# Performance work log

Measured on AMD Instinct MI355X. Metric: run time of the kernel, lower is better.

## Reference

```python
import jax, jax.numpy as jnp
import numpy as np
import math

D = 1024
H = 16
HD = D // H
P = 64  # bias_proj_dim
B, N, M = 4, 1024, 2048
EPS_LN = 1e-5
EPS_NORM = 1e-12


def _ln(x, g, b):
    mu = jnp.mean(x, axis=-1, keepdims=True)
    var = jnp.var(x, axis=-1, keepdims=True)
    return (x - mu) * jax.lax.rsqrt(var + EPS_LN) * g + b


def _l2norm_dim1(x):
    # torch F.normalize(x, p=2) default dim=1 -> normalize over the sequence axis
    n = jnp.sqrt(jnp.sum(x * x, axis=1, keepdims=True))
    return x / jnp.maximum(n, EPS_NORM)


def setup_inputs() -> dict:
    key = jax.random.key(0)
    ks = jax.random.split(key, 16)
    s = 1.0 / math.sqrt(D)
    inp = {
        'dataset_features': jax.random.normal(ks[0], (B, N, D), jnp.float32),
        'visual_features': jax.random.normal(ks[1], (B, M, D), jnp.float32),
        # linear weights stored as (in, out): y = x @ W + b
        'wq_w': jax.random.normal(ks[2], (D, D), jnp.float32) * s,
        'wq_b': jnp.zeros((D,), jnp.float32),
        'wk_w': jax.random.normal(ks[3], (D, D), jnp.float32) * s,
        'wk_b': jnp.zeros((D,), jnp.float32),
        'wv_w': jax.random.normal(ks[4], (D, D), jnp.float32) * s,
        'wv_b': jnp.zeros((D,), jnp.float32),
        'wo_w': jax.random.normal(ks[5], (D, D), jnp.float32) * s,
        'wo_b': jnp.zeros((D,), jnp.float32),
        'gq_w': jax.random.normal(ks[6], (D, P), jnp.float32) * s,
        'gq_b': jnp.zeros((P,), jnp.float32),
        'gk_w': jax.random.normal(ks[7], (D, P), jnp.float32) * s,
        'gk_b': jnp.zeros((P,), jnp.float32),
        'pos_scale': jnp.asarray(2.0, jnp.float32),
        'neg_scale': jnp.asarray(50.0, jnp.float32),
        'attn_logit_scale': jnp.asarray(math.log(10.0), jnp.float32),
        'ln_q_g': jnp.ones((D,), jnp.float32),
        'ln_q_b': jnp.zeros((D,), jnp.float32),
        'ln_kv_g': jnp.ones((D,), jnp.float32),
        'ln_kv_b': jnp.zeros((D,), jnp.float32),
        'ln_out_g': jnp.ones((D,), jnp.float32),
        'ln_out_b': jnp.zeros((D,), jnp.float32),
        'ff1_w': jax.random.normal(ks[8], (D, 2 * D), jnp.float32) * s,
        'ff1_b': jnp.zeros((2 * D,), jnp.float32),
        'ff2_w': jax.random.normal(ks[9], (2 * D, D), jnp.float32) * (1.0 / math.sqrt(2 * D)),
        'ff2_b': jnp.zeros((D,), jnp.float32),
    }
    return inp


def reference(dataset_features, visual_features, wq_w, wq_b, wk_w, wk_b, wv_w, wv_b,
              wo_w, wo_b, gq_w, gq_b, gk_w, gk_b, pos_scale, neg_scale,
              attn_logit_scale, ln_q_g, ln_q_b, ln_kv_g, ln_kv_b, ln_out_g, ln_out_b,
              ff1_w, ff1_b, ff2_w, ff2_b):
    residual = dataset_features
    q_in = _ln(dataset_features, ln_q_g, ln_q_b)   # [B,N,D]
    kv_in = _ln(visual_features, ln_kv_g, ln_kv_b)  # [B,M,D]

    geo_q = _l2norm_dim1(q_in @ gq_w + gq_b)   # [B,N,P], normalized over N
    geo_k = _l2norm_dim1(kv_in @ gk_w + gk_b)  # [B,M,P], normalized over M
    bias_raw = jnp.einsum('bnp,bmp->bnm', geo_q, geo_k)  # [B,N,M]
    full_bias = jax.nn.relu(bias_raw) * pos_scale - jax.nn.relu(-bias_raw) * neg_scale

    q = (q_in @ wq_w + wq_b).reshape(B, N, H, HD).transpose(0, 2, 1, 3)   # [B,H,N,hd]
    k = (kv_in @ wk_w + wk_b).reshape(B, M, H, HD).transpose(0, 2, 1, 3)  # [B,H,M,hd]
    v = (kv_in @ wv_w + wv_b).reshape(B, M, H, HD).transpose(0, 2, 1, 3)

    logits = jnp.einsum('bhnd,bhmd->bhnm', q, k) / math.sqrt(HD)
    logits = logits * jnp.exp(attn_logit_scale)
    scores = logits + full_bias[:, None, :, :]
    attn = jax.nn.softmax(scores, axis=-1)
    out = jnp.einsum('bhnm,bhmd->bhnd', attn, v).transpose(0, 2, 1, 3).reshape(B, N, D)
    out = out @ wo_w + wo_b
    out = residual + out

    residual = out
    h = _ln(out, ln_out_g, ln_out_b)
    ff = jax.nn.gelu(h @ ff1_w + ff1_b, approximate=False) @ ff2_w + ff2_b
    return residual + ff
```

## Files before the change

### kernel.cpp

```cpp
#include <hip/hip_runtime.h>


typedef __bf16 bf16x8 __attribute__((ext_vector_type(8)));
typedef float  f32x4  __attribute__((ext_vector_type(4)));

__device__ inline f32x4 mfma16(bf16x8 a, bf16x8 b, f32x4 c) {
  return __builtin_amdgcn_mfma_f32_16x16x32_bf16(a, b, c, 0, 0, 0);
}

__device__ inline void glds16(const void* g, void* l) {
  __builtin_amdgcn_global_load_lds(
      (const __attribute__((address_space(1))) void*)g,
      (__attribute__((address_space(3))) void*)l, 16, 0, 0);
}

__device__ inline int swz(int row, int col) {
  return row * 64 + ((((col >> 3) ^ (row & 7)) << 3) | (col & 7));
}

#define DB 1024
#define DH 16
#define DHD 64
#define DP 64
#define NB 4
#define NN 1024
#define NM 2048

__global__ __launch_bounds__(256) void k_transpose_all(
    const float* __restrict__ w0, const float* __restrict__ w1,
    const float* __restrict__ w2, const float* __restrict__ w3,
    const float* __restrict__ f1, const float* __restrict__ f2,
    const float* __restrict__ g0, const float* __restrict__ g1,
    __bf16* __restrict__ o0, __bf16* __restrict__ o1,
    __bf16* __restrict__ o2, __bf16* __restrict__ o3,
    __bf16* __restrict__ of1, __bf16* __restrict__ of2,
    __bf16* __restrict__ og0, __bf16* __restrict__ og1) {
  __shared__ float tile[32][33];
  int id = blockIdx.x;
  const float* in;
  __bf16* out;
  int K, O, x, y;
  if (id < 4096) {
    int mi = id >> 10, r = id & 1023;
    in = mi == 0 ? w0 : mi == 1 ? w1 : mi == 2 ? w2 : w3;
    out = mi == 0 ? o0 : mi == 1 ? o1 : mi == 2 ? o2 : o3;
    K = 1024; O = 1024; x = r & 31; y = r >> 5;
  } else if (id < 6144) {
    int r = id - 4096; in = f1; out = of1; K = 1024; O = 2048; x = r & 63; y = r >> 6;
  } else if (id < 8192) {
    int r = id - 6144; in = f2; out = of2; K = 2048; O = 1024; x = r & 31; y = r >> 5;
  } else if (id < 8256) {
    int r = id - 8192; in = g0; out = og0; K = 1024; O = 64; x = r & 1; y = r >> 1;
  } else {
    int r = id - 8256; in = g1; out = og1; K = 1024; O = 64; x = r & 1; y = r >> 1;
  }
  int k0 = y * 32, o0c = x * 32;
  int tx = threadIdx.x & 31, ty = threadIdx.x >> 5;
#pragma unroll
  for (int r = ty; r < 32; r += 8)
    tile[r][tx] = in[(size_t)(k0 + r) * O + (o0c + tx)];
  __syncthreads();
#pragma unroll
  for (int r = ty; r < 32; r += 8)
    out[(size_t)(o0c + r) * K + (k0 + tx)] = (__bf16)tile[tx][r];
}

__device__ inline void ln_body(const float* __restrict__ x,
                               const float* __restrict__ g,
                               const float* __restrict__ bb,
                               __bf16* __restrict__ y, size_t row) {
  int t = threadIdx.x;
  float4 v = ((const float4*)(x + row * 1024))[t];
  float s = v.x + v.y + v.z + v.w;
  float ss = v.x * v.x + v.y * v.y + v.z * v.z + v.w * v.w;
#pragma unroll
  for (int o = 32; o; o >>= 1) {
    s += __shfl_down(s, o, 64);
    ss += __shfl_down(ss, o, 64);
  }
  __shared__ float r1[4], r2[4];
  if ((t & 63) == 0) { r1[t >> 6] = s; r2[t >> 6] = ss; }
  __syncthreads();
  s = r1[0] + r1[1] + r1[2] + r1[3];
  ss = r2[0] + r2[1] + r2[2] + r2[3];
  float mu = s * (1.f / 1024.f);
  float rstd = rsqrtf(ss * (1.f / 1024.f) - mu * mu + 1e-5f);
  float4 gv = ((const float4*)g)[t];
  float4 bv = ((const float4*)bb)[t];
  __bf16* yr = y + row * 1024 + t * 4;
  yr[0] = (__bf16)((v.x - mu) * rstd * gv.x + bv.x);
  yr[1] = (__bf16)((v.y - mu) * rstd * gv.y + bv.y);
  yr[2] = (__bf16)((v.z - mu) * rstd * gv.z + bv.z);
  yr[3] = (__bf16)((v.w - mu) * rstd * gv.w + bv.w);
}

__global__ __launch_bounds__(256) void k_layernorm(
    const float* __restrict__ x, const float* __restrict__ g,
    const float* __restrict__ bb, __bf16* __restrict__ y) {
  ln_body(x, g, bb, y, blockIdx.x);
}

__global__ __launch_bounds__(256) void k_layernorm2(
    const float* __restrict__ x1, const float* __restrict__ g1,
    const float* __restrict__ b1, __bf16* __restrict__ y1,
    const float* __restrict__ x2, const float* __restrict__ g2,
    const float* __restrict__ b2, __bf16* __restrict__ y2) {
  int row = blockIdx.x;
  if (row < 4096) ln_body(x1, g1, b1, y1, row);
  else ln_body(x2, g2, b2, y2, row - 4096);
}

__global__ __launch_bounds__(256) void k_geo(
    const __bf16* __restrict__ qin, const __bf16* __restrict__ kvin,
    const __bf16* __restrict__ gqw, const __bf16* __restrict__ gkw,
    const float* __restrict__ gqb, const float* __restrict__ gkb,
    __bf16* __restrict__ geoq, __bf16* __restrict__ geok) {
  const int blk = blockIdx.x;
  const bool isq = blk < 128;
  const __bf16* A = isq ? qin : kvin;
  const __bf16* Bt = isq ? gqw : gkw;
  const float* bias = isq ? gqb : gkb;
  __bf16* C = isq ? geoq : geok;
  const int row0 = (isq ? blk : blk - 128) * 32;
  __shared__ __align__(16) __bf16 As[32][72], Bs[64][72];
  const int t = threadIdx.x, lane = t & 63, w = t >> 6;
  const int quad = lane >> 4, l15 = lane & 15;
  const int wr = w >> 1, wc = w & 1;
  const int sr = t >> 3, skc = (t & 7) * 8;
  const __bf16* aP = A + (size_t)(row0 + sr) * 1024 + skc;
  const __bf16* bP0 = Bt + (size_t)sr * 1024 + skc;
  const __bf16* bP1 = Bt + (size_t)(sr + 32) * 1024 + skc;
  bf16x8 av = *(const bf16x8*)aP;
  bf16x8 bv0 = *(const bf16x8*)bP0;
  bf16x8 bv1 = *(const bf16x8*)bP1;
  f32x4 acc[2] = {};
  for (int k0 = 0; k0 < 1024; k0 += 64) {
    __syncthreads();
    *(bf16x8*)&As[sr][skc] = av;
    *(bf16x8*)&Bs[sr][skc] = bv0;
    *(bf16x8*)&Bs[sr + 32][skc] = bv1;
    __syncthreads();
    if (k0 + 64 < 1024) {
      av = *(const bf16x8*)(aP + k0 + 64);
      bv0 = *(const bf16x8*)(bP0 + k0 + 64);
      bv1 = *(const bf16x8*)(bP1 + k0 + 64);
    }
#pragma unroll
    for (int ks = 0; ks < 2; ks++) {
      bf16x8 af = *(const bf16x8*)&As[wr * 16 + l15][ks * 32 + quad * 8];
#pragma unroll
      for (int ct = 0; ct < 2; ct++) {
        bf16x8 bfr = *(const bf16x8*)&Bs[wc * 32 + ct * 16 + l15][ks * 32 + quad * 8];
        acc[ct] = mfma16(af, bfr, acc[ct]);
      }
    }
  }
#pragma unroll
  for (int ct = 0; ct < 2; ct++) {
    int col = wc * 32 + ct * 16 + l15;
    float bc = bias[col];
#pragma unroll
    for (int i = 0; i < 4; i++) {
      int row = row0 + wr * 16 + quad * 4 + i;
      C[(size_t)row * 64 + col] = (__bf16)(acc[ct][i] + bc);
    }
  }
}

__global__ __launch_bounds__(256) void k_l2sum(
    const __bf16* __restrict__ gq, const __bf16* __restrict__ gk,
    float* __restrict__ sums) {
  int chunk = blockIdx.x, b = blockIdx.y, z = blockIdx.z;
  if (z == 0 && chunk >= 8) return;
  const __bf16* src = z ? gk : gq;
  int rows = z ? 2048 : 1024;
  const unsigned* base = (const unsigned*)(src + (size_t)b * rows * 64) + chunk * 128 * 32;
  int t = threadIdx.x, c = t & 31, ro = t >> 5;
  float s0 = 0.f, s1 = 0.f;
  for (int r = ro; r < 128; r += 8) {
    unsigned u = base[r * 32 + c];
    float f0 = __uint_as_float(u << 16);
    float f1 = __uint_as_float(u & 0xffff0000u);
    s0 += f0 * f0;
    s1 += f1 * f1;
  }
  __shared__ float ls[64];
  if (t < 64) ls[t] = 0.f;
  __syncthreads();
  atomicAdd(&ls[c * 2], s0);
  atomicAdd(&ls[c * 2 + 1], s1);
  __syncthreads();
  if (t < 64) atomicAdd(&sums[z * 256 + b * 64 + t], ls[t]);
}

__global__ __launch_bounds__(256) void k_l2scale(
    __bf16* __restrict__ gk, const float* __restrict__ sums) {
  int chunk = blockIdx.x, b = blockIdx.y;
  unsigned* base = (unsigned*)(gk + (size_t)b * 2048 * 64) + chunk * 128 * 32;
  int t = threadIdx.x, c = t & 31, ro = t >> 5;
  float sq0 = sums[b * 64 + c * 2], sq1 = sums[b * 64 + c * 2 + 1];
  float sk0 = sums[256 + b * 64 + c * 2], sk1 = sums[256 + b * 64 + c * 2 + 1];
  float m0 = 1.f / (fmaxf(sqrtf(sq0), 1e-12f) * fmaxf(sqrtf(sk0), 1e-12f));
  float m1 = 1.f / (fmaxf(sqrtf(sq1), 1e-12f) * fmaxf(sqrtf(sk1), 1e-12f));
  for (int r = ro; r < 128; r += 8) {
    unsigned u = base[r * 32 + c];
    float f0 = __uint_as_float(u << 16) * m0;
    float f1 = __uint_as_float(u & 0xffff0000u) * m1;
    unsigned short h0 = __builtin_bit_cast(unsigned short, (__bf16)f0);
    unsigned short h1 = __builtin_bit_cast(unsigned short, (__bf16)f1);
    base[r * 32 + c] = (unsigned)h0 | ((unsigned)h1 << 16);
  }
}

__global__ __launch_bounds__(256, 3) void k_qkv(
    const __bf16* __restrict__ qin, const __bf16* __restrict__ kvin,
    const __bf16* __restrict__ twq, const __bf16* __restrict__ twk,
    const __bf16* __restrict__ twv, const float* __restrict__ qbias,
    const float* __restrict__ kbias, const float* __restrict__ vbias,
    __bf16* __restrict__ qb, __bf16* __restrict__ kb, __bf16* __restrict__ vtb) {
  int id = blockIdx.x;
  const __bf16 *A, *Bt;
  const float* bias;
  __bf16* C;
  int my, nx, Ndim;
  bool rowbias;
  if (id < 256) {
    A = qin; Bt = twq; bias = qbias; C = qb;
    nx = id & 7; my = id >> 3; Ndim = 1024; rowbias = false;
  } else if (id < 768) {
    id -= 256;
    A = kvin; Bt = twk; bias = kbias; C = kb;
    nx = id & 7; my = id >> 3; Ndim = 1024; rowbias = false;
  } else {
    id -= 768;
    A = twv; Bt = kvin; bias = vbias; C = vtb;
    nx = id & 63; my = id >> 6; Ndim = 8192; rowbias = true;
  }
  const int Kdim = 1024;
  __shared__ __align__(16) __bf16 As[128 * 32];
  __shared__ __align__(16) __bf16 Bs[128 * 32];
  const int m0 = my * 128, n0 = nx * 128;
  const int t = threadIdx.x, lane = t & 63, w = t >> 6;
  const int quad = lane >> 4, l15 = lane & 15;
  const int wr = w >> 1, wc = w & 1;
  const int srow = lane >> 2, scol = (lane & 3) * 8;
  const __bf16* aS0 = A + (size_t)(m0 + w * 32 + srow) * Kdim + scol;
  const __bf16* bS0 = Bt + (size_t)(n0 + w * 32 + srow) * Kdim + scol;
  const size_t K16 = (size_t)16 * Kdim;
  __bf16* lA0 = &As[(w * 32) * 32];
  __bf16* lB0 = &Bs[(w * 32) * 32];

  f32x4 acc[4][4] = {};
  for (int k0 = 0; k0 < Kdim; k0 += 32) {
    __syncthreads();
    glds16(aS0 + k0, lA0);
    glds16(aS0 + K16 + k0, lA0 + 16 * 32);
    glds16(bS0 + k0, lB0);
    glds16(bS0 + K16 + k0, lB0 + 16 * 32);
    __syncthreads();
    bf16x8 af[4], bg[4];
#pragma unroll
    for (int rt = 0; rt < 4; rt++)
      af[rt] = *(const bf16x8*)&As[(wr * 64 + rt * 16 + l15) * 32 + quad * 8];
#pragma unroll
    for (int ct = 0; ct < 4; ct++)
      bg[ct] = *(const bf16x8*)&Bs[(wc * 64 + ct * 16 + l15) * 32 + quad * 8];
#pragma unroll
    for (int rt = 0; rt < 4; rt++)
#pragma unroll
      for (int ct = 0; ct < 4; ct++)
        acc[rt][ct] = mfma16(af[rt], bg[ct], acc[rt][ct]);
  }
#pragma unroll
  for (int rt = 0; rt < 4; rt++) {
    int row = m0 + wr * 64 + rt * 16 + quad * 4;
#pragma unroll
    for (int ct = 0; ct < 4; ct++) {
      int col = n0 + wc * 64 + ct * 16 + l15;
      float bcol = rowbias ? 0.f : bias[col];
#pragma unroll
      for (int i = 0; i < 4; i++) {
        float vv = acc[rt][ct][i] + (rowbias ? bias[row + i] : bcol);
        C[(size_t)(row + i) * Ndim + col] = (__bf16)vv;
      }
    }
  }
}

__global__ __launch_bounds__(256, 3) void k_gemm128g(
    const __bf16* __restrict__ A, const __bf16* __restrict__ Bt,
    const float* __restrict__ bias, __bf16* __restrict__ Cout,
    int Ndim, int Kdim) {
  __shared__ __align__(16) __bf16 As[128 * 32];
  __shared__ __align__(16) __bf16 Bs[128 * 32];
  const int m0 = blockIdx.y * 128, n0 = blockIdx.x * 128;
  const int t = threadIdx.x, lane = t & 63, w = t >> 6;
  const int quad = lane >> 4, l15 = lane & 15;
  const int wr = w >> 1, wc = w & 1;
  const int srow = lane >> 2, scol = (lane & 3) * 8;
  const __bf16* aS0 = A + (size_t)(m0 + w * 32 + srow) * Kdim + scol;
  const __bf16* bS0 = Bt + (size_t)(n0 + w * 32 + srow) * Kdim + scol;
  const size_t K16 = (size_t)16 * Kdim;
  __bf16* lA0 = &As[(w * 32) * 32];
  __bf16* lB0 = &Bs[(w * 32) * 32];

  f32x4 acc[4][4] = {};
  for (int k0 = 0; k0 < Kdim; k0 += 32) {
    __syncthreads();
    glds16(aS0 + k0, lA0);
    glds16(aS0 + K16 + k0, lA0 + 16 * 32);
    glds16(bS0 + k0, lB0);
    glds16(bS0 + K16 + k0, lB0 + 16 * 32);
    __syncthreads();
    bf16x8 af[4], bg[4];
#pragma unroll
    for (int rt = 0; rt < 4; rt++)
      af[rt] = *(const bf16x8*)&As[(wr * 64 + rt * 16 + l15) * 32 + quad * 8];
#pragma unroll
    for (int ct = 0; ct < 4; ct++)
      bg[ct] = *(const bf16x8*)&Bs[(wc * 64 + ct * 16 + l15) * 32 + quad * 8];
#pragma unroll
    for (int rt = 0; rt < 4; rt++)
#pragma unroll
      for (int ct = 0; ct < 4; ct++)
        acc[rt][ct] = mfma16(af[rt], bg[ct], acc[rt][ct]);
  }
#pragma unroll
  for (int rt = 0; rt < 4; rt++) {
    int row = m0 + wr * 64 + rt * 16 + quad * 4;
#pragma unroll
    for (int ct = 0; ct < 4; ct++) {
      int col = n0 + wc * 64 + ct * 16 + l15;
      float bcol = bias[col];
#pragma unroll
      for (int i = 0; i < 4; i++) {
        float vv = acc[rt][ct][i] + bcol;
        Cout[(size_t)(row + i) * Ndim + col] =
            (__bf16)(0.5f * vv * (1.f + erff(vv * 0.70710678118f)));
      }
    }
  }
}

__global__ __launch_bounds__(256, 2) void k_gemmn64(
    const __bf16* __restrict__ A, const __bf16* __restrict__ Bt,
    const float* __restrict__ bias, const float* __restrict__ resid,
    float* __restrict__ Cout, int Ndim, int Kdim) {
  __shared__ __align__(16) __bf16 As[128 * 32];
  __shared__ __align__(16) __bf16 Bs[64 * 32];
  const int m0 = blockIdx.y * 128, n0 = blockIdx.x * 64;
  const int t = threadIdx.x, lane = t & 63, w = t >> 6;
  const int quad = lane >> 4, l15 = lane & 15;
  const int wr = w >> 1, wc = w & 1;
  const int srow = lane >> 2, scol = (lane & 3) * 8;
  const __bf16* aS0 = A + (size_t)(m0 + w * 32 + srow) * Kdim + scol;
  const __bf16* bS0 = Bt + (size_t)(n0 + w * 16 + srow) * Kdim + scol;
  const size_t K16 = (size_t)16 * Kdim;
  __bf16* lA0 = &As[(w * 32) * 32];
  __bf16* lB0 = &Bs[(w * 16) * 32];

  f32x4 acc[4][2] = {};
  for (int k0 = 0; k0 < Kdim; k0 += 32) {
    __syncthreads();
    glds16(aS0 + k0, lA0);
    glds16(aS0 + K16 + k0, lA0 + 16 * 32);
    glds16(bS0 + k0, lB0);
    __syncthreads();
    bf16x8 af[4], bg[2];
#pragma unroll
    for (int rt = 0; rt < 4; rt++)
      af[rt] = *(const bf16x8*)&As[(wr * 64 + rt * 16 + l15) * 32 + quad * 8];
#pragma unroll
    for (int ct = 0; ct < 2; ct++)
      bg[ct] = *(const bf16x8*)&Bs[(wc * 32 + ct * 16 + l15) * 32 + quad * 8];
#pragma unroll
    for (int rt = 0; rt < 4; rt++)
#pragma unroll
      for (int ct = 0; ct < 2; ct++)
        acc[rt][ct] = mfma16(af[rt], bg[ct], acc[rt][ct]);
  }
#pragma unroll
  for (int rt = 0; rt < 4; rt++) {
    int row = m0 + wr * 64 + rt * 16 + quad * 4;
#pragma unroll
    for (int ct = 0; ct < 2; ct++) {
      int col = n0 + wc * 32 + ct * 16 + l15;
      float bcol = bias[col];
#pragma unroll
      for (int i = 0; i < 4; i++) {
        size_t idx = (size_t)(row + i) * Ndim + col;
        Cout[idx] = acc[rt][ct][i] + bcol + resid[idx];
      }
    }
  }
}

__global__ __launch_bounds__(256, 2) void k_flash(
    const __bf16* __restrict__ Q, const __bf16* __restrict__ K,
    const __bf16* __restrict__ Vt, const __bf16* __restrict__ Gq,
    const __bf16* __restrict__ Gk, const float* __restrict__ als,
    const float* __restrict__ psc, const float* __restrict__ nsc,
    float* __restrict__ Opart, float* __restrict__ lpart) {
  const int o = blockIdx.x;
  const int bh = o & 63, kv = (o >> 6) & 1, x = o >> 7;
  const int b = bh & 3, h = bh >> 2;
  const int t = threadIdx.x, w = t >> 6, lane = t & 63;
  const int quad = lane >> 4, l15 = lane & 15;
  const int row0 = x * 128 + w * 32;
  const float LOG2E = 1.44269504089f;
  const float sc2 = __expf(als[0]) * 0.125f * LOG2E;
  const float pos2 = psc[0] * LOG2E, neg2 = nsc[0] * LOG2E;

  __shared__ __align__(16) __bf16 Ks[64 * 64];
  __shared__ __align__(16) __bf16 Gs[64 * 64];
  __shared__ __align__(16) __bf16 Vs[64 * 64];
  __shared__ __align__(16) __bf16 plds[4][32 * 64];

  const __bf16* Qb = Q + ((size_t)(b * NN + row0)) * DB + h * DHD;
  const __bf16* Kb = K + ((size_t)b * NM) * DB + h * DHD;
  const __bf16* Vb = Vt + (size_t)(h * DHD) * (NB * NM) + (size_t)b * NM;
  const __bf16* Gqb = Gq + (size_t)(b * NN + row0) * DP;
  const __bf16* Gkb = Gk + (size_t)b * NM * DP;

  const int r0 = t >> 3, ch = t & 7, gc = ch * 8;
  const int sw0 = swz(r0, gc), sw1 = sw0 + 32 * 64;
  const int r1 = r0 + 32;

  bf16x8 qf[2][2], gqf[2][2];
#pragma unroll
  for (int rt = 0; rt < 2; rt++)
#pragma unroll
    for (int ks = 0; ks < 2; ks++) {
      qf[rt][ks] = *(const bf16x8*)(Qb + (size_t)(rt * 16 + l15) * DB + ks * 32 + quad * 8);
      gqf[rt][ks] = *(const bf16x8*)(Gqb + (size_t)(rt * 16 + l15) * DP + ks * 32 + quad * 8);
    }

  const int mlo = kv * 1024;
  bf16x8 kst0 = *(const bf16x8*)(Kb + (size_t)(mlo + r0) * DB + gc);
  bf16x8 kst1 = *(const bf16x8*)(Kb + (size_t)(mlo + r1) * DB + gc);
  bf16x8 gst0 = *(const bf16x8*)(Gkb + (size_t)(mlo + r0) * DP + gc);
  bf16x8 gst1 = *(const bf16x8*)(Gkb + (size_t)(mlo + r1) * DP + gc);
  bf16x8 vst0 = *(const bf16x8*)(Vb + (size_t)r0 * (NB * NM) + mlo + gc);
  bf16x8 vst1 = *(const bf16x8*)(Vb + (size_t)r1 * (NB * NM) + mlo + gc);

  float lrow[2][4] = {};
  f32x4 oacc[2][4] = {};
  f32x4 z4 = {0.f, 0.f, 0.f, 0.f};

  for (int m0 = mlo; m0 < mlo + 1024; m0 += 64) {
    __syncthreads();
    *(bf16x8*)&Ks[sw0] = kst0;
    *(bf16x8*)&Ks[sw1] = kst1;
    *(bf16x8*)&Gs[sw0] = gst0;
    *(bf16x8*)&Gs[sw1] = gst1;
    *(bf16x8*)&Vs[sw0] = vst0;
    *(bf16x8*)&Vs[sw1] = vst1;
    __syncthreads();
    if (m0 + 64 < mlo + 1024) {
      kst0 = *(const bf16x8*)(Kb + (size_t)(m0 + 64 + r0) * DB + gc);
      kst1 = *(const bf16x8*)(Kb + (size_t)(m0 + 64 + r1) * DB + gc);
      gst0 = *(const bf16x8*)(Gkb + (size_t)(m0 + 64 + r0) * DP + gc);
      gst1 = *(const bf16x8*)(Gkb + (size_t)(m0 + 64 + r1) * DP + gc);
      vst0 = *(const bf16x8*)(Vb + (size_t)r0 * (NB * NM) + m0 + 64 + gc);
      vst1 = *(const bf16x8*)(Vb + (size_t)r1 * (NB * NM) + m0 + 64 + gc);
    }
    bf16x8 kf[4][2], gkf[4][2];
#pragma unroll
    for (int ct = 0; ct < 4; ct++)
#pragma unroll
      for (int ks = 0; ks < 2; ks++) {
        int off = swz(ct * 16 + l15, ks * 32 + quad * 8);
        kf[ct][ks] = *(const bf16x8*)&Ks[off];
        gkf[ct][ks] = *(const bf16x8*)&Gs[off];
      }
#pragma unroll
    for (int rt = 0; rt < 2; rt++)
#pragma unroll
      for (int ct = 0; ct < 4; ct++) {
        f32x4 s = mfma16(qf[rt][1], kf[ct][1], mfma16(qf[rt][0], kf[ct][0], z4));
        f32x4 bg = mfma16(gqf[rt][1], gkf[ct][1], mfma16(gqf[rt][0], gkf[ct][0], z4));
#pragma unroll
        for (int i = 0; i < 4; i++) {
          float bb = bg[i];
          float scl = bb > 0.f ? pos2 : neg2;
          float p = __builtin_amdgcn_exp2f(fmaf(bb, scl, s[i] * sc2));
          lrow[rt][i] += p;
          plds[w][swz(rt * 16 + quad * 4 + i, ct * 16 + l15)] = (__bf16)p;
        }
      }
    bf16x8 pf[2][2], vf[4][2];
#pragma unroll
    for (int rt = 0; rt < 2; rt++)
#pragma unroll
      for (int ms = 0; ms < 2; ms++)
        pf[rt][ms] = *(const bf16x8*)&plds[w][swz(rt * 16 + l15, ms * 32 + quad * 8)];
#pragma unroll
    for (int dt = 0; dt < 4; dt++)
#pragma unroll
      for (int ms = 0; ms < 2; ms++)
        vf[dt][ms] = *(const bf16x8*)&Vs[swz(dt * 16 + l15, ms * 32 + quad * 8)];
#pragma unroll
    for (int rt = 0; rt < 2; rt++)
#pragma unroll
      for (int dt = 0; dt < 4; dt++) {
        oacc[rt][dt] = mfma16(pf[rt][0], vf[dt][0], oacc[rt][dt]);
        oacc[rt][dt] = mfma16(pf[rt][1], vf[dt][1], oacc[rt][dt]);
      }
  }
  float* op = Opart + ((size_t)kv * NB * NN + b * NN + row0) * DB + h * 64;
  float* lp = lpart + ((size_t)kv * NB * NN + b * NN + row0) * DH + h;
#pragma unroll
  for (int rt = 0; rt < 2; rt++)
#pragma unroll
    for (int i = 0; i < 4; i++) {
      float l = lrow[rt][i];
#pragma unroll
      for (int o2 = 1; o2 < 16; o2 <<= 1) l += __shfl_xor(l, o2, 64);
      int r = rt * 16 + quad * 4 + i;
#pragma unroll
      for (int dt = 0; dt < 4; dt++)
        op[(size_t)r * DB + dt * 16 + l15] = oacc[rt][dt][i];
      if (l15 == 0) lp[(size_t)r * DH] = l;
    }
}

__global__ __launch_bounds__(256) void k_combine(
    const float* __restrict__ Opart, const float* __restrict__ lpart,
    __bf16* __restrict__ attn) {
  const int bn = blockIdx.x;
  const int t = threadIdx.x, c = t * 4, h = c >> 6;
  const float4 o0 = *(const float4*)&Opart[(size_t)bn * DB + c];
  const float4 o1 = *(const float4*)&Opart[((size_t)NB * NN + bn) * DB + c];
  float l0 = lpart[(size_t)bn * DH + h];
  float l1 = lpart[((size_t)NB * NN + bn) * DH + h];
  float inv = 1.f / (l0 + l1);
  __bf16* dst = attn + (size_t)bn * DB + c;
  dst[0] = (__bf16)((o0.x + o1.x) * inv);
  dst[1] = (__bf16)((o0.y + o1.y) * inv);
  dst[2] = (__bf16)((o0.z + o1.z) * inv);
  dst[3] = (__bf16)((o0.w + o1.w) * inv);
}

extern "C" void kernel_launch(void* const* d_in, const int* in_sizes, int n_in,
                              void* d_out, int out_size, void* d_ws, size_t ws_size,
                              hipStream_t stream) {
  const float* dataset = (const float*)d_in[0];
  const float* visual = (const float*)d_in[1];
  const float* wq_w = (const float*)d_in[2];
  const float* wq_b = (const float*)d_in[3];
  const float* wk_w = (const float*)d_in[4];
  const float* wk_b = (const float*)d_in[5];
  const float* wv_w = (const float*)d_in[6];
  const float* wv_b = (const float*)d_in[7];
  const float* wo_w = (const float*)d_in[8];
  const float* wo_b = (const float*)d_in[9];
  const float* gq_w = (const float*)d_in[10];
  const float* gq_b = (const float*)d_in[11];
  const float* gk_w = (const float*)d_in[12];
  const float* gk_b = (const float*)d_in[13];
  const float* pos_scale = (const float*)d_in[14];
  const float* neg_scale = (const float*)d_in[15];
  const float* als = (const float*)d_in[16];
  const float* ln_q_g = (const float*)d_in[17];
  const float* ln_q_b = (const float*)d_in[18];
  const float* ln_kv_g = (const float*)d_in[19];
  const float* ln_kv_b = (const float*)d_in[20];
  const float* ln_out_g = (const float*)d_in[21];
  const float* ln_out_b = (const float*)d_in[22];
  const float* ff1_w = (const float*)d_in[23];
  const float* ff1_b = (const float*)d_in[24];
  const float* ff2_w = (const float*)d_in[25];
  const float* ff2_b = (const float*)d_in[26];

  char* ws = (char*)d_ws;
  size_t off = 0;
  auto alloc = [&](size_t bytes) {
    size_t o = off;
    off += (bytes + 255) & ~(size_t)255;
    return o;
  };
  __bf16* t_wq = (__bf16*)(ws + alloc((size_t)1024 * 1024 * 2));
  __bf16* t_wk = (__bf16*)(ws + alloc((size_t)1024 * 1024 * 2));
  __bf16* t_wv = (__bf16*)(ws + alloc((size_t)1024 * 1024 * 2));
  __bf16* t_wo = (__bf16*)(ws + alloc((size_t)1024 * 1024 * 2));
  __bf16* t_ff1 = (__bf16*)(ws + alloc((size_t)2048 * 1024 * 2));
  __bf16* t_ff2 = (__bf16*)(ws + alloc((size_t)1024 * 2048 * 2));
  __bf16* t_gq = (__bf16*)(ws + alloc((size_t)64 * 1024 * 2));
  __bf16* t_gk = (__bf16*)(ws + alloc((size_t)64 * 1024 * 2));
  size_t qin_off = alloc((size_t)4096 * 1024 * 2);
  size_t kvin_off = alloc((size_t)8192 * 1024 * 2);
  __bf16* qin = (__bf16*)(ws + qin_off);
  __bf16* kvin = (__bf16*)(ws + kvin_off);
  __bf16* geoq = (__bf16*)(ws + alloc((size_t)4096 * 64 * 2));
  __bf16* geok = (__bf16*)(ws + alloc((size_t)8192 * 64 * 2));
  float* sums = (float*)(ws + alloc((size_t)2 * 4 * 64 * 4));
  __bf16* qb = (__bf16*)(ws + alloc((size_t)4096 * 1024 * 2));
  __bf16* kb = (__bf16*)(ws + alloc((size_t)8192 * 1024 * 2));
  __bf16* vtb = (__bf16*)(ws + alloc((size_t)1024 * 8192 * 2));
  __bf16* attn = (__bf16*)(ws + alloc((size_t)4096 * 1024 * 2));
  __bf16* ffh = (__bf16*)(ws + alloc((size_t)4096 * 2048 * 2));
  float* opart = (float*)(ws + alloc((size_t)2 * 4096 * 1024 * 4));
  float* lpart = (float*)(ws + alloc((size_t)2 * 4096 * 16 * 4));
  float* out1 = (float*)(ws + kvin_off);
  __bf16* hbuf = (__bf16*)(ws + qin_off);
  float* outp = (float*)d_out;

  dim3 blk(256);
  k_transpose_all<<<8320, blk, 0, stream>>>(wq_w, wk_w, wv_w, wo_w, ff1_w, ff2_w,
                                            gq_w, gk_w, t_wq, t_wk, t_wv, t_wo,
                                            t_ff1, t_ff2, t_gq, t_gk);
  k_layernorm2<<<12288, blk, 0, stream>>>(dataset, ln_q_g, ln_q_b, qin,
                                          visual, ln_kv_g, ln_kv_b, kvin);
  k_geo<<<384, blk, 0, stream>>>(qin, kvin, t_gq, t_gk, gq_b, gk_b, geoq, geok);
  hipMemsetAsync(sums, 0, 2 * 4 * 64 * 4, stream);
  k_l2sum<<<dim3(16, 4, 2), blk, 0, stream>>>(geoq, geok, sums);
  k_l2scale<<<dim3(16, 4), blk, 0, stream>>>(geok, sums);
  k_qkv<<<1280, blk, 0, stream>>>(qin, kvin, t_wq, t_wk, t_wv,
                                  wq_b, wk_b, wv_b, qb, kb, vtb);
  k_flash<<<1024, blk, 0, stream>>>(qb, kb, vtb, geoq, geok, als,
                                    pos_scale, neg_scale, opart, lpart);
  k_combine<<<4096, blk, 0, stream>>>(opart, lpart, attn);
  k_gemmn64<<<dim3(16, 32), blk, 0, stream>>>(attn, t_wo, wo_b, dataset, out1,
                                              1024, 1024);
  k_layernorm<<<4096, blk, 0, stream>>>(out1, ln_out_g, ln_out_b, hbuf);
  k_gemm128g<<<dim3(16, 32), blk, 0, stream>>>(hbuf, t_ff1, ff1_b, ffh,
                                               2048, 1024);
  k_gemmn64<<<dim3(16, 32), blk, 0, stream>>>(ffh, t_ff2, ff2_b, out1, outp,
                                              1024, 2048);
}
```

Measured before the change: 458.9 us.

## Drop split-KV in flash attention, normalize in-kernel, transpose score MFMA

Removes the two-way split over the key axis so each block processes all 2048 keys and normalizes the output directly to bf16. This eliminates the fp32 partial-output buffers and the separate combine kernel. The score MFMAs are also swapped (K as A operand) so each lane holds four consecutive keys and can write P with a packed 4-element store, and the row-sum reduction needs fewer shuffles. The grid halves to 512 blocks, which lowers parallelism on a large-CU GPU and makes each block's serial loop twice as long.

```diff
diff --git a/kernel.cpp b/kernel.cpp
--- a/kernel.cpp
+++ b/kernel.cpp
@@ -2,6 +2,7 @@
 
 
 typedef __bf16 bf16x8 __attribute__((ext_vector_type(8)));
+typedef __bf16 bf16x4 __attribute__((ext_vector_type(4)));
 typedef float  f32x4  __attribute__((ext_vector_type(4)));
 
 __device__ inline f32x4 mfma16(bf16x8 a, bf16x8 b, f32x4 c) {
@@ -400,9 +401,9 @@
     const __bf16* __restrict__ Vt, const __bf16* __restrict__ Gq,
     const __bf16* __restrict__ Gk, const float* __restrict__ als,
     const float* __restrict__ psc, const float* __restrict__ nsc,
-    float* __restrict__ Opart, float* __restrict__ lpart) {
+    __bf16* __restrict__ Out) {
   const int o = blockIdx.x;
-  const int bh = o & 63, kv = (o >> 6) & 1, x = o >> 7;
+  const int bh = o & 63, x = o >> 6;
   const int b = bh & 3, h = bh >> 2;
   const int t = threadIdx.x, w = t >> 6, lane = t & 63;
   const int quad = lane >> 4, l15 = lane & 15;
@@ -414,7 +415,7 @@
   __shared__ __align__(16) __bf16 Ks[64 * 64];
   __shared__ __align__(16) __bf16 Gs[64 * 64];
   __shared__ __align__(16) __bf16 Vs[64 * 64];
-  __shared__ __align__(16) __bf16 plds[4][32 * 64];
+  __shared__ __align__(16) __bf16 Ps[4][32 * 64];
 
   const __bf16* Qb = Q + ((size_t)(b * NN + row0)) * DB + h * DHD;
   const __bf16* Kb = K + ((size_t)b * NM) * DB + h * DHD;
@@ -422,7 +423,7 @@
   const __bf16* Gqb = Gq + (size_t)(b * NN + row0) * DP;
   const __bf16* Gkb = Gk + (size_t)b * NM * DP;
 
-  const int r0 = t >> 3, ch = t & 7, gc = ch * 8;
+  const int r0 = t >> 3, gc = (t & 7) * 8;
   const int sw0 = swz(r0, gc), sw1 = sw0 + 32 * 64;
   const int r1 = r0 + 32;
 
@@ -435,19 +436,18 @@
       gqf[rt][ks] = *(const bf16x8*)(Gqb + (size_t)(rt * 16 + l15) * DP + ks * 32 + quad * 8);
     }
 
-  const int mlo = kv * 1024;
-  bf16x8 kst0 = *(const bf16x8*)(Kb + (size_t)(mlo + r0) * DB + gc);
-  bf16x8 kst1 = *(const bf16x8*)(Kb + (size_t)(mlo + r1) * DB + gc);
-  bf16x8 gst0 = *(const bf16x8*)(Gkb + (size_t)(mlo + r0) * DP + gc);
-  bf16x8 gst1 = *(const bf16x8*)(Gkb + (size_t)(mlo + r1) * DP + gc);
-  bf16x8 vst0 = *(const bf16x8*)(Vb + (size_t)r0 * (NB * NM) + mlo + gc);
-  bf16x8 vst1 = *(const bf16x8*)(Vb + (size_t)r1 * (NB * NM) + mlo + gc);
-
-  float lrow[2][4] = {};
+  bf16x8 kst0 = *(const bf16x8*)(Kb + (size_t)r0 * DB + gc);
+  bf16x8 kst1 = *(const bf16x8*)(Kb + (size_t)r1 * DB + gc);
+  bf16x8 gst0 = *(const bf16x8*)(Gkb + (size_t)r0 * DP + gc);
+  bf16x8 gst1 = *(const bf16x8*)(Gkb + (size_t)r1 * DP + gc);
+  bf16x8 vst0 = *(const bf16x8*)(Vb + (size_t)r0 * (NB * NM) + gc);
+  bf16x8 vst1 = *(const bf16x8*)(Vb + (size_t)r1 * (NB * NM) + gc);
+
+  float lrowq[2] = {};
   f32x4 oacc[2][4] = {};
   f32x4 z4 = {0.f, 0.f, 0.f, 0.f};
 
-  for (int m0 = mlo; m0 < mlo + 1024; m0 += 64) {
+  for (int m0 = 0; m0 < NM; m0 += 64) {
     __syncthreads();
     *(bf16x8*)&Ks[sw0] = kst0;
     *(bf16x8*)&Ks[sw1] = kst1;
@@ -456,7 +456,7 @@
     *(bf16x8*)&Vs[sw0] = vst0;
     *(bf16x8*)&Vs[sw1] = vst1;
     __syncthreads();
-    if (m0 + 64 < mlo + 1024) {
+    if (m0 + 64 < NM) {
       kst0 = *(const bf16x8*)(Kb + (size_t)(m0 + 64 + r0) * DB + gc);
       kst1 = *(const bf16x8*)(Kb + (size_t)(m0 + 64 + r1) * DB + gc);
       gst0 = *(const bf16x8*)(Gkb + (size_t)(m0 + 64 + r0) * DP + gc);
@@ -474,26 +474,30 @@
         gkf[ct][ks] = *(const bf16x8*)&Gs[off];
       }
 #pragma unroll
-    for (int rt = 0; rt < 2; rt++)
-#pragma unroll
-      for (int ct = 0; ct < 4; ct++) {
-        f32x4 s = mfma16(qf[rt][1], kf[ct][1], mfma16(qf[rt][0], kf[ct][0], z4));
-        f32x4 bg = mfma16(gqf[rt][1], gkf[ct][1], mfma16(gqf[rt][0], gkf[ct][0], z4));
+    for (int ct = 0; ct < 4; ct++)
+#pragma unroll
+      for (int rt = 0; rt < 2; rt++) {
+        f32x4 s = mfma16(kf[ct][1], qf[rt][1], mfma16(kf[ct][0], qf[rt][0], z4));
+        f32x4 bg = mfma16(gkf[ct][1], gqf[rt][1], mfma16(gkf[ct][0], gqf[rt][0], z4));
+        bf16x4 pk;
+        float part = 0.f;
 #pragma unroll
         for (int i = 0; i < 4; i++) {
           float bb = bg[i];
           float scl = bb > 0.f ? pos2 : neg2;
           float p = __builtin_amdgcn_exp2f(fmaf(bb, scl, s[i] * sc2));
-          lrow[rt][i] += p;
-          plds[w][swz(rt * 16 + quad * 4 + i, ct * 16 + l15)] = (__bf16)p;
+          part += p;
+          pk[i] = (__bf16)p;
         }
+        lrowq[rt] += part;
+        *(bf16x4*)&Ps[w][swz(rt * 16 + l15, ct * 16 + quad * 4)] = pk;
       }
     bf16x8 pf[2][2], vf[4][2];
 #pragma unroll
     for (int rt = 0; rt < 2; rt++)
 #pragma unroll
       for (int ms = 0; ms < 2; ms++)
-        pf[rt][ms] = *(const bf16x8*)&plds[w][swz(rt * 16 + l15, ms * 32 + quad * 8)];
+        pf[rt][ms] = *(const bf16x8*)&Ps[w][swz(rt * 16 + l15, ms * 32 + quad * 8)];
 #pragma unroll
     for (int dt = 0; dt < 4; dt++)
 #pragma unroll
@@ -507,38 +511,25 @@
         oacc[rt][dt] = mfma16(pf[rt][1], vf[dt][1], oacc[rt][dt]);
       }
   }
-  float* op = Opart + ((size_t)kv * NB * NN + b * NN + row0) * DB + h * 64;
-  float* lp = lpart + ((size_t)kv * NB * NN + b * NN + row0) * DH + h;
+  float ltot[2];
+#pragma unroll
+  for (int rt = 0; rt < 2; rt++) {
+    float l = lrowq[rt];
+    l += __shfl_xor(l, 16, 64);
+    l += __shfl_xor(l, 32, 64);
+    ltot[rt] = l;
+  }
 #pragma unroll
   for (int rt = 0; rt < 2; rt++)
 #pragma unroll
     for (int i = 0; i < 4; i++) {
-      float l = lrow[rt][i];
-#pragma unroll
-      for (int o2 = 1; o2 < 16; o2 <<= 1) l += __shfl_xor(l, o2, 64);
-      int r = rt * 16 + quad * 4 + i;
+      float li = __shfl(ltot[rt], quad * 4 + i, 64);
+      float inv = 1.f / li;
 #pragma unroll
       for (int dt = 0; dt < 4; dt++)
-        op[(size_t)r * DB + dt * 16 + l15] = oacc[rt][dt][i];
-      if (l15 == 0) lp[(size_t)r * DH] = l;
-    }
-}
-
-__global__ __launch_bounds__(256) void k_combine(
-    const float* __restrict__ Opart, const float* __restrict__ lpart,
-    __bf16* __restrict__ attn) {
-  const int bn = blockIdx.x;
-  const int t = threadIdx.x, c = t * 4, h = c >> 6;
-  const float4 o0 = *(const float4*)&Opart[(size_t)bn * DB + c];
-  const float4 o1 = *(const float4*)&Opart[((size_t)NB * NN + bn) * DB + c];
-  float l0 = lpart[(size_t)bn * DH + h];
-  float l1 = lpart[((size_t)NB * NN + bn) * DH + h];
-  float inv = 1.f / (l0 + l1);
-  __bf16* dst = attn + (size_t)bn * DB + c;
-  dst[0] = (__bf16)((o0.x + o1.x) * inv);
-  dst[1] = (__bf16)((o0.y + o1.y) * inv);
-  dst[2] = (__bf16)((o0.z + o1.z) * inv);
-  dst[3] = (__bf16)((o0.w + o1.w) * inv);
+        Out[(size_t)(b * NN + row0 + rt * 16 + quad * 4 + i) * DB + h * DHD + dt * 16 + l15] =
+            (__bf16)(oacc[rt][dt][i] * inv);
+    }
 }
 
 extern "C" void kernel_launch(void* const* d_in, const int* in_sizes, int n_in,
@@ -599,8 +590,6 @@
   __bf16* vtb = (__bf16*)(ws + alloc((size_t)1024 * 8192 * 2));
   __bf16* attn = (__bf16*)(ws + alloc((size_t)4096 * 1024 * 2));
   __bf16* ffh = (__bf16*)(ws + alloc((size_t)4096 * 2048 * 2));
-  float* opart = (float*)(ws + alloc((size_t)2 * 4096 * 1024 * 4));
-  float* lpart = (float*)(ws + alloc((size_t)2 * 4096 * 16 * 4));
   float* out1 = (float*)(ws + kvin_off);
   __bf16* hbuf = (__bf16*)(ws + qin_off);
   float* outp = (float*)d_out;
@@ -617,9 +606,8 @@
   k_l2scale<<<dim3(16, 4), blk, 0, stream>>>(geok, sums);
   k_qkv<<<1280, blk, 0, stream>>>(qin, kvin, t_wq, t_wk, t_wv,
                                   wq_b, wk_b, wv_b, qb, kb, vtb);
-  k_flash<<<1024, blk, 0, stream>>>(qb, kb, vtb, geoq, geok, als,
-                                    pos_scale, neg_scale, opart, lpart);
-  k_combine<<<4096, blk, 0, stream>>>(opart, lpart, attn);
+  k_flash<<<512, blk, 0, stream>>>(qb, kb, vtb, geoq, geok, als,
+                                   pos_scale, neg_scale, attn);
   k_gemmn64<<<dim3(16, 32), blk, 0, stream>>>(attn, t_wo, wo_b, dataset, out1,
                                               1024, 1024);
   k_layernorm<<<4096, blk, 0, stream>>>(out1, ln_out_g, ln_out_b, hbuf);
```

Result: faster. 435.1 us (-5.2%).
